# Kernel tuning notes

Measured on AMD Instinct MI355X. Metric: run time of the kernel, lower is better.

The kernel has to match this reference:

```python
import jax, jax.numpy as jnp
import numpy as np

N_FFT = 4096
HOP = 1024
WIN = 300          # wiener_win_len (frames per independent Wiener chunk)
EPS = 1e-10
SCALE_FACTOR = 10.0


def hann(n):
    # torch.hann_window (periodic)
    return 0.5 * (1.0 - jnp.cos(2.0 * jnp.pi * jnp.arange(n) / n))


def stft(x, window):
    # x: (N, C, T) -> complex (N, C, B, F), center=True, reflect pad, onesided
    pad = N_FFT // 2
    xp = jnp.pad(x, ((0, 0), (0, 0), (pad, pad)), mode='reflect')
    n_frames = 1 + (xp.shape[-1] - N_FFT) // HOP
    idx = jnp.arange(n_frames)[:, None] * HOP + jnp.arange(N_FFT)[None, :]
    frames = xp[..., idx] * window                      # (N,C,F,n_fft)
    spec = jnp.fft.rfft(frames, axis=-1)                # (N,C,F,B)
    return jnp.swapaxes(spec, -1, -2)                   # (N,C,B,F)


def istft(spec, window, length):
    # spec: (..., B, F) complex -> (..., length) real; center=True inverse
    frames = jnp.fft.irfft(jnp.swapaxes(spec, -1, -2), n=N_FFT, axis=-1) * window
    n_frames = frames.shape[-2]
    out_len = N_FFT + HOP * (n_frames - 1)
    idx = jnp.arange(n_frames)[:, None] * HOP + jnp.arange(N_FFT)[None, :]
    out = jnp.zeros(frames.shape[:-2] + (out_len,), frames.dtype).at[..., idx].add(frames)
    wsum = jnp.zeros((out_len,), frames.dtype).at[idx].add(
        jnp.broadcast_to(window ** 2, idx.shape))
    out = out / jnp.where(wsum > 1e-11, wsum, 1.0)
    pad = N_FFT // 2
    return out[..., pad:pad + length]


def wiener_chunk(v, x, niter):
    # openunmix.filtering.wiener (softmask=False, residual=False) on one chunk.
    # v: (T, B, C, S) real target magnitudes; x: (T, B, C) complex mix STFT.
    phase = jnp.exp(1j * jnp.angle(x))                  # mixture phase init
    y = (v * phase[..., None]).astype(jnp.complex64)    # (T,B,C,S)
    max_abs = jnp.maximum(1.0, jnp.max(jnp.abs(x)) / SCALE_FACTOR)
    x = x / max_abs
    y = y / max_abs
    C = x.shape[-1]
    reg = np.sqrt(EPS) * jnp.eye(C, dtype=jnp.complex64)
    for _ in range(niter):  # expectation_maximization, one pass per iter
        psd = jnp.mean(jnp.abs(y) ** 2, axis=2)         # (T,B,S) channel-avg PSD
        # spatial covariance per bin/source, normalized by eps + sum_t psd
        R = jnp.einsum('tbcs,tbds->bcds', y, jnp.conj(y))
        R = R / (EPS + jnp.sum(psd, axis=0))[:, None, None, :]
        Cxx = reg + jnp.einsum('tbs,bcds->tbcd', psd.astype(jnp.complex64), R)
        inv = jnp.linalg.inv(Cxx)                       # (T,B,C,C)
        gain = jnp.einsum('bacs,tbcd->tbads', R, inv) * psd[:, :, None, None, :]
        y = jnp.einsum('tbacs,tbc->tbas', gain, x)      # (T,B,C,S)
    return y * max_abs


def setup_inputs() -> dict:
    key = jax.random.key(0)
    k1, k2 = jax.random.split(key)
    audio = jax.random.normal(k1, (2, 2, 613376), dtype=jnp.float32)
    W = jax.random.normal(k2, (4, 2049), dtype=jnp.float32)  # per-target per-bin mask logits
    return {'audio': audio, 'W': W, 'niter': 1}


def reference(audio, W, niter):
    window = hann(N_FFT).astype(audio.dtype)
    mix = stft(audio, window)                           # (N,C,B,F) complex
    X = jnp.abs(mix)                                    # ComplexNorm power=1
    # target models (stand-in: per-bin sigmoid masks); input detached as in torch
    Xd = jax.lax.stop_gradient(X)
    masks = jax.nn.sigmoid(W)                           # (S,B)
    specs = Xd[..., None] * jnp.transpose(masks)[None, None, :, None, :]  # (N,C,B,F,S)
    v = jnp.transpose(specs, (0, 3, 2, 1, 4))           # (N,F,B,C,S)
    xm = jnp.transpose(mix, (0, 3, 2, 1))               # (N,F,B,C)
    N, F, B, C = xm.shape
    S = v.shape[-1]
    n_chunks = F // WIN
    vc = v.reshape(N, n_chunks, WIN, B, C, S)
    xc = xm.reshape(N, n_chunks, WIN, B, C)
    wfun = lambda vv, xx: wiener_chunk(vv, xx, niter)
    yc = jax.vmap(jax.vmap(wfun))(vc, xc)               # (N,chunks,T,B,C,S)
    y = yc.reshape(N, F, B, C, S)
    y = jnp.transpose(y, (0, 4, 3, 2, 1))               # (N,S,C,B,F)
    estimates = istft(y, window, audio.shape[-1])       # (N,S,C,T)
    return estimates
```

## Files before the change

### kernel.cpp

```cpp
#include <hip/hip_runtime.h>
#include <math.h>

#define TLEN 613376
#define OLEN 617472
#define NFR  600
#define NB   2049
#define PI_F  3.14159265358979323846f
#define PI2_F 6.28318530717958647693f
#define PHYS(i) ((i) + ((i) >> 4))

__device__ __forceinline__ float winf(int j) {
  return 0.5f - 0.5f * __cosf(1.5339807878856412e-3f * (float)j);
}

__device__ __forceinline__ float wsum_at(int m) {
  int f_max = m >> 10; if (f_max > 599) f_max = 599;
  int f_min = (m - 3072) >> 10; if (f_min < 0) f_min = 0;
  float ws = 0.f;
  for (int f2 = f_min; f2 <= f_max; ++f2) {
    float w = winf(m - (f2 << 10));
    ws += w * w;
  }
  return (ws > 1e-11f) ? ws : 1.0f;
}

__device__ __forceinline__ float reflect_load(const float* __restrict__ x, int pos) {
  int k = pos - 2048;
  if (k < 0) k = -k;
  else if (k >= TLEN) k = 2 * TLEN - 2 - k;
  return x[k];
}

__device__ __forceinline__ float2 cmul(float2 a, float2 b) {
  return make_float2(a.x * b.x - a.y * b.y, a.x * b.y + a.y * b.x);
}
__device__ __forceinline__ float2 cadd(float2 a, float2 b) { return make_float2(a.x + b.x, a.y + b.y); }
__device__ __forceinline__ float2 csub(float2 a, float2 b) { return make_float2(a.x - b.x, a.y - b.y); }
template<int SGN>
__device__ __forceinline__ float2 muli(float2 a) {
  return (SGN > 0) ? make_float2(-a.y, a.x) : make_float2(a.y, -a.x);
}

template<int SGN>
__device__ __forceinline__ void fft4(float2 v[4]) {
  float2 t0 = cadd(v[0], v[2]), t1 = csub(v[0], v[2]);
  float2 t2 = cadd(v[1], v[3]), t3 = csub(v[1], v[3]);
  float2 it3 = muli<SGN>(t3);
  v[0] = cadd(t0, t2); v[2] = csub(t0, t2);
  v[1] = cadd(t1, it3); v[3] = csub(t1, it3);
}

template<int SGN>
__device__ __forceinline__ void fft8(float2 v[8]) {
  const float C = 0.70710678118654752440f;
  const float s = (SGN > 0) ? 1.0f : -1.0f;
  float2 t0 = cadd(v[0], v[4]), t1 = csub(v[0], v[4]);
  float2 t2 = cadd(v[2], v[6]), t3 = csub(v[2], v[6]);
  float2 e0 = cadd(t0, t2), e2 = csub(t0, t2);
  float2 it3 = muli<SGN>(t3);
  float2 e1 = cadd(t1, it3), e3 = csub(t1, it3);
  t0 = cadd(v[1], v[5]); t1 = csub(v[1], v[5]);
  t2 = cadd(v[3], v[7]); t3 = csub(v[3], v[7]);
  float2 o0 = cadd(t0, t2), o2 = csub(t0, t2);
  it3 = muli<SGN>(t3);
  float2 o1 = cadd(t1, it3), o3 = csub(t1, it3);
  float2 o1w = make_float2(C * (o1.x - s * o1.y), C * (o1.y + s * o1.x));
  float2 o2w = muli<SGN>(o2);
  float2 o3w = make_float2(C * (-o3.x - s * o3.y), C * (-o3.y + s * o3.x));
  v[0] = cadd(e0, o0);  v[4] = csub(e0, o0);
  v[1] = cadd(e1, o1w); v[5] = csub(e1, o1w);
  v[2] = cadd(e2, o2w); v[6] = csub(e2, o2w);
  v[3] = cadd(e3, o3w); v[7] = csub(e3, o3w);
}

template<int SGN>
__device__ __forceinline__ void twiddle8(float2 v[8], float ang) {
  float sn, cs;
  __sincosf((SGN > 0) ? ang : -ang, &sn, &cs);
  float2 w1 = make_float2(cs, sn);
  float2 w = w1;
  v[1] = cmul(v[1], w);
#pragma unroll
  for (int r = 2; r < 8; ++r) { w = cmul(w, w1); v[r] = cmul(v[r], w); }
}

template<int SGN>
__device__ __forceinline__ void fft2048_mid(float2* lds, float2 v[8], int tid) {
  fft8<SGN>(v);
#pragma unroll
  for (int r = 0; r < 8; ++r) { int i = tid * 8 + r; lds[PHYS(i)] = v[r]; }
  __syncthreads();
#pragma unroll
  for (int r = 0; r < 8; ++r) v[r] = lds[PHYS(tid + 256 * r)];
  twiddle8<SGN>(v, PI2_F * (1.0f / 64.0f) * (float)(tid & 7));
  fft8<SGN>(v);
  __syncthreads();
#pragma unroll
  for (int r = 0; r < 8; ++r) { int i = ((tid >> 3) << 6) + (tid & 7) + 8 * r; lds[PHYS(i)] = v[r]; }
  __syncthreads();
#pragma unroll
  for (int r = 0; r < 8; ++r) v[r] = lds[PHYS(tid + 256 * r)];
  twiddle8<SGN>(v, PI2_F * (1.0f / 512.0f) * (float)(tid & 63));
  fft8<SGN>(v);
  __syncthreads();
#pragma unroll
  for (int r = 0; r < 8; ++r) { int i = ((tid >> 6) << 9) + (tid & 63) + 64 * r; lds[PHYS(i)] = v[r]; }
  __syncthreads();
}

template<int SGN>
__device__ __forceinline__ void fft2048_last(const float2* lds, int jj, float2 u[4]) {
#pragma unroll
  for (int r = 0; r < 4; ++r) u[r] = lds[PHYS(jj + 512 * r)];
  float sn, cs;
  float ang = PI2_F * (1.0f / 2048.0f) * (float)jj;
  __sincosf((SGN > 0) ? ang : -ang, &sn, &cs);
  float2 w1 = make_float2(cs, sn);
  float2 w2 = cmul(w1, w1);
  float2 w3 = cmul(w2, w1);
  u[1] = cmul(u[1], w1); u[2] = cmul(u[2], w2); u[3] = cmul(u[3], w3);
  fft4<SGN>(u);
}

__global__ __launch_bounds__(256, 6) void stft_kernel(const float* __restrict__ audio,
                                                      float2* __restrict__ X) {
  __shared__ float2 lds[2176];
  int bid = blockIdx.x;
  int w  = (bid & 7) * 300 + (bid >> 3);
  int f  = w % NFR;
  int nc = w / NFR;
  const float* x = audio + (size_t)nc * TLEN;
  int tid = threadIdx.x;
  int base = f * 1024;
  float2 v[8];
#pragma unroll
  for (int r = 0; r < 8; ++r) {
    int k = tid + 256 * r;
    int j0 = 2 * k;
    v[r] = make_float2(reflect_load(x, base + j0)     * winf(j0),
                       reflect_load(x, base + j0 + 1) * winf(j0 + 1));
  }
  fft2048_mid<-1>(lds, v, tid);
  fft2048_last<-1>(lds, tid,        v);
  fft2048_last<-1>(lds, tid + 256,  v + 4);
  __syncthreads();
#pragma unroll
  for (int r = 0; r < 4; ++r) lds[PHYS(tid + 512 * r)] = v[r];
#pragma unroll
  for (int r = 0; r < 4; ++r) lds[PHYS(tid + 256 + 512 * r)] = v[4 + r];
  __syncthreads();
  float2* out = X + ((size_t)nc * NFR + f) * NB;
  float sn0, cs0;
  __sincosf(-PI_F * (float)tid * (1.0f / 2048.0f), &sn0, &cs0);
  float2 ph = make_float2(cs0, sn0);
  const float2 rot = make_float2(0.92387953251128675613f, -0.38268343236508977173f);
#pragma unroll
  for (int r = 0; r < 9; ++r) {
    int k = tid + 256 * r;
    if (k <= 2048) {
      float2 Zk = lds[PHYS(k & 2047)];
      float2 Zm = lds[PHYS((2048 - k) & 2047)];
      float Ex = 0.5f * (Zk.x + Zm.x), Ey = 0.5f * (Zk.y - Zm.y);
      float Dx = 0.5f * (Zk.x - Zm.x), Dy = 0.5f * (Zk.y + Zm.y);
      float Ox = Dy, Oy = -Dx;
      out[k] = make_float2(Ex + Ox * ph.x - Oy * ph.y, Ey + Ox * ph.y + Oy * ph.x);
    }
    ph = cmul(ph, rot);
  }
}

__global__ __launch_bounds__(256) void stats_kernel(const float2* __restrict__ X,
                                                    float* __restrict__ stats4,
                                                    unsigned int* __restrict__ maxsq) {
  __shared__ unsigned int sm;
  if (threadIdx.x == 0) sm = 0u;
  __syncthreads();
  int b = blockIdx.x * 256 + threadIdx.x;
  bool ok = (b < NB);
  int g = blockIdx.y;
  int n = g >> 1, chunk = g & 1;
  int t0 = blockIdx.z * 75;
  const float2* X0 = X + ((size_t)(n * 2 + 0) * NFR + chunk * 300 + t0) * NB + (ok ? b : 0);
  const float2* X1 = X + ((size_t)(n * 2 + 1) * NFR + chunk * 300 + t0) * NB + (ok ? b : 0);
  float s00 = 0.f, s11 = 0.f, sre = 0.f, sim = 0.f, lmax = 0.f;
  if (ok) {
    for (int t = 0; t < 75; ++t) {
      float2 a = X0[(size_t)t * NB];
      float2 c = X1[(size_t)t * NB];
      float pa = a.x * a.x + a.y * a.y;
      float pc = c.x * c.x + c.y * c.y;
      s00 += pa; s11 += pc;
      sre += a.x * c.x + a.y * c.y;
      sim += a.y * c.x - a.x * c.y;
      lmax = fmaxf(lmax, fmaxf(pa, pc));
    }
  }
  atomicMax(&sm, __float_as_uint(lmax));
  __syncthreads();
  if (threadIdx.x == 0) atomicMax(&maxsq[g], sm);
  if (ok) {
    float* sp = stats4 + ((size_t)g * NB + b) * 4;
    unsafeAtomicAdd(sp + 0, s00);
    unsafeAtomicAdd(sp + 1, s11);
    unsafeAtomicAdd(sp + 2, sre);
    unsafeAtomicAdd(sp + 3, sim);
  }
}

__global__ __launch_bounds__(256) void alpha_kernel(const float* __restrict__ Wmask,
                                                    const float4* __restrict__ stats4,
                                                    const unsigned int* __restrict__ maxsq,
                                                    float* __restrict__ alpha,
                                                    float* __restrict__ Ksum) {
  int idx = blockIdx.x * 256 + threadIdx.x;
  if (idx >= 4 * NB) return;
  int b = idx % NB;
  int g = idx / NB;
  float ma2 = fmaxf(1.0f, __uint_as_float(maxsq[g]) * 0.01f);
  float4 s4 = stats4[(size_t)g * NB + b];
  float P = 0.5f * (s4.x + s4.y) / ma2;
  float K = 0.f;
#pragma unroll
  for (int s = 0; s < 4; ++s) {
    float mv = 1.0f / (1.0f + expf(-Wmask[s * NB + b]));
    float m2 = mv * mv;
    float a = (m2 * m2) / (1e-10f + m2 * P);
    alpha[(size_t)(g * 4 + s) * NB + b] = a;
    K += a;
  }
  Ksum[(size_t)g * NB + b] = K;
}

__global__ __launch_bounds__(256) void wiener_kernel(const float2* __restrict__ X,
                                                     const float4* __restrict__ stats4,
                                                     const float* __restrict__ Ksum,
                                                     const unsigned int* __restrict__ maxsq,
                                                     float2* __restrict__ Wc) {
  int idx = blockIdx.x * 256 + threadIdx.x;
  if (idx >= 4 * 300 * NB) return;
  int b = idx % NB;
  int gt = idx / NB;
  int t = gt % 300;
  int g = gt / 300;
  int n = g >> 1, chunk = g & 1;
  int f = chunk * 300 + t;
  float ima2 = 1.0f / fmaxf(1.0f, __uint_as_float(maxsq[g]) * 0.01f);
  float4 s4 = stats4[(size_t)g * NB + b];
  float g00 = s4.x * ima2, g11 = s4.y * ima2, gre = s4.z * ima2, gim = s4.w * ima2;
  float K = Ksum[(size_t)g * NB + b];
  float2 x0 = X[((size_t)(n * 2 + 0) * NFR + f) * NB + b];
  float2 x1 = X[((size_t)(n * 2 + 1) * NFR + f) * NB + b];
  float ph = 0.5f * ((x0.x * x0.x + x0.y * x0.y) + (x1.x * x1.x + x1.y * x1.y)) * ima2;
  float pk = ph * K;
  float M00 = 1e-5f + pk * g00;
  float M11 = 1e-5f + pk * g11;
  float Mre = pk * gre, Mim = pk * gim;
  float det = M00 * M11 - (Mre * Mre + Mim * Mim);
  float sc = ph / det;
  float u0x = M11 * x0.x - (Mre * x1.x - Mim * x1.y);
  float u0y = M11 * x0.y - (Mre * x1.y + Mim * x1.x);
  float u1x = M00 * x1.x - (Mre * x0.x + Mim * x0.y);
  float u1y = M00 * x1.y - (Mre * x0.y - Mim * x0.x);
  float w0x = g00 * u0x + (gre * u1x - gim * u1y);
  float w0y = g00 * u0y + (gre * u1y + gim * u1x);
  float w1x = (gre * u0x + gim * u0y) + g11 * u1x;
  float w1y = (gre * u0y - gim * u0x) + g11 * u1y;
  float2* out = Wc + ((size_t)(n * NFR + f) * 2) * NB + b;
  out[0]  = make_float2(w0x * sc, w0y * sc);
  out[NB] = make_float2(w1x * sc, w1y * sc);
}

template<int MODE>
__global__ __launch_bounds__(256, 6) void istft_pass_kernel(const float2* __restrict__ Wc,
                                                            const float* __restrict__ alpha,
                                                            float* __restrict__ accum,
                                                            float* __restrict__ out,
                                                            int pass) {
  __shared__ float2 lds[2176];
  int bid = blockIdx.x;
  int w = (bid & 7) * 300 + (bid >> 3);
  int member = w & 7;
  int grp = w >> 3;
  int fi = grp % 150;
  int n  = grp / 150;
  int s = member >> 1;
  int c = member & 1;
  int plane = n * 8 + s * 2 + c;
  int f = 4 * fi + pass;
  int g = n * 2 + (f >= 300 ? 1 : 0);
  int tid = threadIdx.x;
  const float2* Wrow = Wc + ((size_t)(n * NFR + f) * 2 + c) * NB;
  const float*  arow = alpha + (size_t)(g * 4 + s) * NB;
  float* acc = accum + (size_t)plane * OLEN + (size_t)f * 1024;

  float2 pre[8];
  if (MODE >= 1) {
#pragma unroll
    for (int half = 0; half < 2; ++half) {
#pragma unroll
      for (int r = 0; r < 4; ++r) {
        int m = tid + 256 * half + 512 * r;
        pre[half * 4 + r] = *(const float2*)&acc[2 * m];
      }
    }
  }

  float2 v[8];
  float sn0, cs0;
  __sincosf(PI_F * (float)tid * (1.0f / 2048.0f), &sn0, &cs0);
  float2 ph = make_float2(cs0, sn0);
  const float2 rot = make_float2(0.92387953251128675613f, 0.38268343236508977173f);
#pragma unroll
  for (int r = 0; r < 8; ++r) {
    int k = tid + 256 * r;
    float ak = arow[k];
    float2 sk = Wrow[k]; sk.x *= ak; sk.y *= ak;
    int rk = 2048 - k;
    float am = arow[rk];
    float2 sv = Wrow[rk]; sv.x *= am; sv.y *= am;
    float Ex = 0.5f * (sk.x + sv.x), Ey = 0.5f * (sk.y - sv.y);
    float Dx = 0.5f * (sk.x - sv.x), Dy = 0.5f * (sk.y + sv.y);
    float Ox = Dx * ph.x - Dy * ph.y, Oy = Dx * ph.y + Dy * ph.x;
    v[r] = make_float2(Ex - Oy, Ey + Ox);
    ph = cmul(ph, rot);
  }
  fft2048_mid<1>(lds, v, tid);
  float* outp = out + (size_t)plane * TLEN;
  const float scale = 1.0f / 2048.0f;
#pragma unroll
  for (int half = 0; half < 2; ++half) {
    int jj = tid + 256 * half;
    float2 u[4];
    fft2048_last<1>(lds, jj, u);
#pragma unroll
    for (int r = 0; r < 4; ++r) {
      int m = jj + 512 * r;
      int j0 = 2 * m;
      float2 val = make_float2(u[r].x * scale * winf(j0),
                               u[r].y * scale * winf(j0 + 1));
      float2* p = (float2*)&acc[j0];
      if (MODE == 0) {
        *p = val;
      } else if (MODE == 1) {
        float2 o = pre[half * 4 + r];
        val.x += o.x; val.y += o.y;
        *p = val;
      } else {
        int gm = f * 1024 + j0;
        if (gm < 615424) {
          float2 o = pre[half * 4 + r];
          val.x += o.x; val.y += o.y;
          float i0, i1;
          if (gm >= 3072 && gm + 1 < 614400) {
            i0 = 0.66666666666666667f; i1 = i0;
          } else {
            i0 = 1.0f / wsum_at(gm); i1 = 1.0f / wsum_at(gm + 1);
          }
          float2* po = (float2*)&outp[gm - 2048];
          *po = make_float2(val.x * i0, val.y * i1);
        }
      }
    }
  }
  if (MODE == 0 && fi == 149) {
    float* tail = accum + (size_t)plane * OLEN + 614400;
    for (int i = tid; i < OLEN - 614400; i += 256) tail[i] = 0.f;
  }
  if (MODE == 2 && fi == 0) {
    float* accp = accum + (size_t)plane * OLEN;
    for (int m = 2048 + tid; m < 3072; m += 256) {
      outp[m - 2048] = accp[m] / wsum_at(m);
    }
  }
}

extern "C" void kernel_launch(void* const* d_in, const int* in_sizes, int n_in,
                              void* d_out, int out_size, void* d_ws, size_t ws_size,
                              hipStream_t stream) {
  const float* audio = (const float*)d_in[0];
  const float* Wmask = (const float*)d_in[1];
  float* out = (float*)d_out;

  char* ws = (char*)d_ws;
  const size_t off_stats4 = 0;
  const size_t off_maxsq  = 131136;
  const size_t zero_span  = 131200;
  const size_t off_X      = zero_span;
  const size_t off_Wc     = off_X + 39340800;
  const size_t off_accum  = off_Wc + 39340800;
  const size_t off_alpha  = off_accum + 39518208;
  const size_t off_Ksum   = off_alpha + 131136;

  float*        stats4f = (float*)(ws + off_stats4);
  float4*       stats4  = (float4*)(ws + off_stats4);
  unsigned int* maxsq   = (unsigned int*)(ws + off_maxsq);
  float2*       X       = (float2*)(ws + off_X);
  float2*       Wc      = (float2*)(ws + off_Wc);
  float*        accum   = (float*)(ws + off_accum);
  float*        alpha   = (float*)(ws + off_alpha);
  float*        Ksum    = (float*)(ws + off_Ksum);

  hipMemsetAsync(ws, 0, zero_span, stream);

  stft_kernel<<<2400, 256, 0, stream>>>(audio, X);
  stats_kernel<<<dim3(9, 4, 4), 256, 0, stream>>>(X, stats4f, maxsq);
  alpha_kernel<<<(4 * NB + 255) / 256, 256, 0, stream>>>(Wmask, stats4, maxsq, alpha, Ksum);
  wiener_kernel<<<(4 * 300 * NB + 255) / 256, 256, 0, stream>>>(X, stats4, Ksum, maxsq, Wc);
  istft_pass_kernel<0><<<2400, 256, 0, stream>>>(Wc, alpha, accum, out, 0);
  istft_pass_kernel<1><<<2400, 256, 0, stream>>>(Wc, alpha, accum, out, 1);
  istft_pass_kernel<1><<<2400, 256, 0, stream>>>(Wc, alpha, accum, out, 2);
  istft_pass_kernel<2><<<2400, 256, 0, stream>>>(Wc, alpha, accum, out, 3);
}
```

Before: 199.1 us.

## Fuse Wiener filter evaluation into iSTFT passes, drop Wc intermediate buffer

Removes the standalone wiener_kernel and its ~39MB Wc intermediate. Each iSTFT block now recomputes the 2x2 Wiener solve per bin from X, stats4 and Ksum directly. This avoids writing and re-reading Wc through global memory and saves one launch. The cost is recomputation: the work for both channels is repeated per source (4x), which adds registers, so launch bounds drop to 4 waves and the loop unroll is reduced.

```diff
diff --git a/kernel.cpp b/kernel.cpp
--- a/kernel.cpp
+++ b/kernel.cpp
@@ -231,25 +231,17 @@
   Ksum[(size_t)g * NB + b] = K;
 }
 
-__global__ __launch_bounds__(256) void wiener_kernel(const float2* __restrict__ X,
-                                                     const float4* __restrict__ stats4,
-                                                     const float* __restrict__ Ksum,
-                                                     const unsigned int* __restrict__ maxsq,
-                                                     float2* __restrict__ Wc) {
-  int idx = blockIdx.x * 256 + threadIdx.x;
-  if (idx >= 4 * 300 * NB) return;
-  int b = idx % NB;
-  int gt = idx / NB;
-  int t = gt % 300;
-  int g = gt / 300;
-  int n = g >> 1, chunk = g & 1;
-  int f = chunk * 300 + t;
-  float ima2 = 1.0f / fmaxf(1.0f, __uint_as_float(maxsq[g]) * 0.01f);
-  float4 s4 = stats4[(size_t)g * NB + b];
+__device__ __forceinline__ float2 wiener_eval(int k, int c,
+                                              const float2* __restrict__ X0row,
+                                              const float2* __restrict__ X1row,
+                                              const float4* __restrict__ s4row,
+                                              const float* __restrict__ Krow,
+                                              float ima2) {
+  float4 s4 = s4row[k];
   float g00 = s4.x * ima2, g11 = s4.y * ima2, gre = s4.z * ima2, gim = s4.w * ima2;
-  float K = Ksum[(size_t)g * NB + b];
-  float2 x0 = X[((size_t)(n * 2 + 0) * NFR + f) * NB + b];
-  float2 x1 = X[((size_t)(n * 2 + 1) * NFR + f) * NB + b];
+  float K = Krow[k];
+  float2 x0 = X0row[k];
+  float2 x1 = X1row[k];
   float ph = 0.5f * ((x0.x * x0.x + x0.y * x0.y) + (x1.x * x1.x + x1.y * x1.y)) * ima2;
   float pk = ph * K;
   float M00 = 1e-5f + pk * g00;
@@ -261,17 +253,22 @@
   float u0y = M11 * x0.y - (Mre * x1.y + Mim * x1.x);
   float u1x = M00 * x1.x - (Mre * x0.x + Mim * x0.y);
   float u1y = M00 * x1.y - (Mre * x0.y - Mim * x0.x);
-  float w0x = g00 * u0x + (gre * u1x - gim * u1y);
-  float w0y = g00 * u0y + (gre * u1y + gim * u1x);
-  float w1x = (gre * u0x + gim * u0y) + g11 * u1x;
-  float w1y = (gre * u0y - gim * u0x) + g11 * u1y;
-  float2* out = Wc + ((size_t)(n * NFR + f) * 2) * NB + b;
-  out[0]  = make_float2(w0x * sc, w0y * sc);
-  out[NB] = make_float2(w1x * sc, w1y * sc);
+  float wx, wy;
+  if (c == 0) {
+    wx = g00 * u0x + (gre * u1x - gim * u1y);
+    wy = g00 * u0y + (gre * u1y + gim * u1x);
+  } else {
+    wx = (gre * u0x + gim * u0y) + g11 * u1x;
+    wy = (gre * u0y - gim * u0x) + g11 * u1y;
+  }
+  return make_float2(wx * sc, wy * sc);
 }
 
 template<int MODE>
-__global__ __launch_bounds__(256, 6) void istft_pass_kernel(const float2* __restrict__ Wc,
+__global__ __launch_bounds__(256, 4) void istft_pass_kernel(const float2* __restrict__ X,
+                                                            const float4* __restrict__ stats4,
+                                                            const float* __restrict__ Ksum,
+                                                            const unsigned int* __restrict__ maxsq,
                                                             const float* __restrict__ alpha,
                                                             float* __restrict__ accum,
                                                             float* __restrict__ out,
@@ -289,8 +286,12 @@
   int f = 4 * fi + pass;
   int g = n * 2 + (f >= 300 ? 1 : 0);
   int tid = threadIdx.x;
-  const float2* Wrow = Wc + ((size_t)(n * NFR + f) * 2 + c) * NB;
-  const float*  arow = alpha + (size_t)(g * 4 + s) * NB;
+  const float2* X0row = X + ((size_t)(n * 2 + 0) * NFR + f) * NB;
+  const float2* X1row = X + ((size_t)(n * 2 + 1) * NFR + f) * NB;
+  const float4* s4row = stats4 + (size_t)g * NB;
+  const float*  Krow  = Ksum + (size_t)g * NB;
+  const float*  arow  = alpha + (size_t)(g * 4 + s) * NB;
+  float ima2 = 1.0f / fmaxf(1.0f, __uint_as_float(maxsq[g]) * 0.01f);
   float* acc = accum + (size_t)plane * OLEN + (size_t)f * 1024;
 
   float2 pre[8];
@@ -310,14 +311,16 @@
   __sincosf(PI_F * (float)tid * (1.0f / 2048.0f), &sn0, &cs0);
   float2 ph = make_float2(cs0, sn0);
   const float2 rot = make_float2(0.92387953251128675613f, 0.38268343236508977173f);
-#pragma unroll
+#pragma unroll 4
   for (int r = 0; r < 8; ++r) {
     int k = tid + 256 * r;
     float ak = arow[k];
-    float2 sk = Wrow[k]; sk.x *= ak; sk.y *= ak;
+    float2 sk = wiener_eval(k, c, X0row, X1row, s4row, Krow, ima2);
+    sk.x *= ak; sk.y *= ak;
     int rk = 2048 - k;
     float am = arow[rk];
-    float2 sv = Wrow[rk]; sv.x *= am; sv.y *= am;
+    float2 sv = wiener_eval(rk, c, X0row, X1row, s4row, Krow, ima2);
+    sv.x *= am; sv.y *= am;
     float Ex = 0.5f * (sk.x + sv.x), Ey = 0.5f * (sk.y - sv.y);
     float Dx = 0.5f * (sk.x - sv.x), Dy = 0.5f * (sk.y + sv.y);
     float Ox = Dx * ph.x - Dy * ph.y, Oy = Dx * ph.y + Dy * ph.x;
@@ -386,8 +389,7 @@
   const size_t off_maxsq  = 131136;
   const size_t zero_span  = 131200;
   const size_t off_X      = zero_span;
-  const size_t off_Wc     = off_X + 39340800;
-  const size_t off_accum  = off_Wc + 39340800;
+  const size_t off_accum  = off_X + 39340800;
   const size_t off_alpha  = off_accum + 39518208;
   const size_t off_Ksum   = off_alpha + 131136;
 
@@ -395,7 +397,6 @@
   float4*       stats4  = (float4*)(ws + off_stats4);
   unsigned int* maxsq   = (unsigned int*)(ws + off_maxsq);
   float2*       X       = (float2*)(ws + off_X);
-  float2*       Wc      = (float2*)(ws + off_Wc);
   float*        accum   = (float*)(ws + off_accum);
   float*        alpha   = (float*)(ws + off_alpha);
   float*        Ksum    = (float*)(ws + off_Ksum);
@@ -405,9 +406,8 @@
   stft_kernel<<<2400, 256, 0, stream>>>(audio, X);
   stats_kernel<<<dim3(9, 4, 4), 256, 0, stream>>>(X, stats4f, maxsq);
   alpha_kernel<<<(4 * NB + 255) / 256, 256, 0, stream>>>(Wmask, stats4, maxsq, alpha, Ksum);
-  wiener_kernel<<<(4 * 300 * NB + 255) / 256, 256, 0, stream>>>(X, stats4, Ksum, maxsq, Wc);
-  istft_pass_kernel<0><<<2400, 256, 0, stream>>>(Wc, alpha, accum, out, 0);
-  istft_pass_kernel<1><<<2400, 256, 0, stream>>>(Wc, alpha, accum, out, 1);
-  istft_pass_kernel<1><<<2400, 256, 0, stream>>>(Wc, alpha, accum, out, 2);
-  istft_pass_kernel<2><<<2400, 256, 0, stream>>>(Wc, alpha, accum, out, 3);
-}
+  istft_pass_kernel<0><<<2400, 256, 0, stream>>>(X, stats4, Ksum, maxsq, alpha, accum, out, 0);
+  istft_pass_kernel<1><<<2400, 256, 0, stream>>>(X, stats4, Ksum, maxsq, alpha, accum, out, 1);
+  istft_pass_kernel<1><<<2400, 256, 0, stream>>>(X, stats4, Ksum, maxsq, alpha, accum, out, 2);
+  istft_pass_kernel<2><<<2400, 256, 0, stream>>>(X, stats4, Ksum, maxsq, alpha, accum, out, 3);
+}
```

After: 354.2 us. 77.9% more time.

## Replace four-pass iSTFT overlap-add with single atomic-add kernel

Applied to the files above, without the earlier changes.

Merges the four sequential iSTFT pass launches and the intermediate accumulation buffer into one kernel that applies window normalization per sample and atomically adds into a zeroed output. This removes the read-modify-write of the accum buffer, the extra launches and the edge-fixup logic. In exchange it adds a full output memset and two float atomics per output sample, with overlapping frames contending on the same addresses, and makes summation order nondeterministic.

```diff
diff --git a/kernel.cpp b/kernel.cpp
--- a/kernel.cpp
+++ b/kernel.cpp
@@ -2,7 +2,6 @@
 #include <math.h>
 
 #define TLEN 613376
-#define OLEN 617472
 #define NFR  600
 #define NB   2049
 #define PI_F  3.14159265358979323846f
@@ -270,17 +269,16 @@
   out[NB] = make_float2(w1x * sc, w1y * sc);
 }
 
-template<int MODE>
-__global__ __launch_bounds__(256, 6) void istft_pass_kernel(const float2* __restrict__ Wc,
-                                                            const float* __restrict__ alpha,
-                                                            float* __restrict__ accum,
-                                                            float* __restrict__ out,
-                                                            int pass) {
+__global__ __launch_bounds__(256, 6) void istft_atomic_kernel(const float2* __restrict__ Wc,
+                                                              const float* __restrict__ alpha,
+                                                              float* __restrict__ out) {
   __shared__ float2 lds[2176];
   int bid = blockIdx.x;
-  int w = (bid & 7) * 300 + (bid >> 3);
+  int w = (bid & 7) * 1200 + (bid >> 3);
   int member = w & 7;
-  int grp = w >> 3;
+  int rest = w >> 3;
+  int pass = rest & 3;
+  int grp = rest >> 2;
   int fi = grp % 150;
   int n  = grp / 150;
   int s = member >> 1;
@@ -291,19 +289,6 @@
   int tid = threadIdx.x;
   const float2* Wrow = Wc + ((size_t)(n * NFR + f) * 2 + c) * NB;
   const float*  arow = alpha + (size_t)(g * 4 + s) * NB;
-  float* acc = accum + (size_t)plane * OLEN + (size_t)f * 1024;
-
-  float2 pre[8];
-  if (MODE >= 1) {
-#pragma unroll
-    for (int half = 0; half < 2; ++half) {
-#pragma unroll
-      for (int r = 0; r < 4; ++r) {
-        int m = tid + 256 * half + 512 * r;
-        pre[half * 4 + r] = *(const float2*)&acc[2 * m];
-      }
-    }
-  }
 
   float2 v[8];
   float sn0, cs0;
@@ -336,40 +321,19 @@
     for (int r = 0; r < 4; ++r) {
       int m = jj + 512 * r;
       int j0 = 2 * m;
-      float2 val = make_float2(u[r].x * scale * winf(j0),
-                               u[r].y * scale * winf(j0 + 1));
-      float2* p = (float2*)&acc[j0];
-      if (MODE == 0) {
-        *p = val;
-      } else if (MODE == 1) {
-        float2 o = pre[half * 4 + r];
-        val.x += o.x; val.y += o.y;
-        *p = val;
-      } else {
-        int gm = f * 1024 + j0;
-        if (gm < 615424) {
-          float2 o = pre[half * 4 + r];
-          val.x += o.x; val.y += o.y;
-          float i0, i1;
-          if (gm >= 3072 && gm + 1 < 614400) {
-            i0 = 0.66666666666666667f; i1 = i0;
-          } else {
-            i0 = 1.0f / wsum_at(gm); i1 = 1.0f / wsum_at(gm + 1);
-          }
-          float2* po = (float2*)&outp[gm - 2048];
-          *po = make_float2(val.x * i0, val.y * i1);
+      int gm = f * 1024 + j0;
+      if (gm >= 2048 && gm < 615424) {
+        float i0, i1;
+        if (gm >= 3072 && gm + 1 < 614400) {
+          i0 = 0.66666666666666667f; i1 = i0;
+        } else {
+          i0 = 1.0f / wsum_at(gm); i1 = 1.0f / wsum_at(gm + 1);
         }
+        float vx = u[r].x * scale * winf(j0)     * i0;
+        float vy = u[r].y * scale * winf(j0 + 1) * i1;
+        unsafeAtomicAdd(&outp[gm - 2048], vx);
+        unsafeAtomicAdd(&outp[gm - 2047], vy);
       }
-    }
-  }
-  if (MODE == 0 && fi == 149) {
-    float* tail = accum + (size_t)plane * OLEN + 614400;
-    for (int i = tid; i < OLEN - 614400; i += 256) tail[i] = 0.f;
-  }
-  if (MODE == 2 && fi == 0) {
-    float* accp = accum + (size_t)plane * OLEN;
-    for (int m = 2048 + tid; m < 3072; m += 256) {
-      outp[m - 2048] = accp[m] / wsum_at(m);
     }
   }
 }
@@ -387,8 +351,7 @@
   const size_t zero_span  = 131200;
   const size_t off_X      = zero_span;
   const size_t off_Wc     = off_X + 39340800;
-  const size_t off_accum  = off_Wc + 39340800;
-  const size_t off_alpha  = off_accum + 39518208;
+  const size_t off_alpha  = off_Wc + 39340800;
   const size_t off_Ksum   = off_alpha + 131136;
 
   float*        stats4f = (float*)(ws + off_stats4);
@@ -396,18 +359,15 @@
   unsigned int* maxsq   = (unsigned int*)(ws + off_maxsq);
   float2*       X       = (float2*)(ws + off_X);
   float2*       Wc      = (float2*)(ws + off_Wc);
-  float*        accum   = (float*)(ws + off_accum);
   float*        alpha   = (float*)(ws + off_alpha);
   float*        Ksum    = (float*)(ws + off_Ksum);
 
   hipMemsetAsync(ws, 0, zero_span, stream);
+  hipMemsetAsync(d_out, 0, out_size, stream);
 
   stft_kernel<<<2400, 256, 0, stream>>>(audio, X);
   stats_kernel<<<dim3(9, 4, 4), 256, 0, stream>>>(X, stats4f, maxsq);
   alpha_kernel<<<(4 * NB + 255) / 256, 256, 0, stream>>>(Wmask, stats4, maxsq, alpha, Ksum);
   wiener_kernel<<<(4 * 300 * NB + 255) / 256, 256, 0, stream>>>(X, stats4, Ksum, maxsq, Wc);
-  istft_pass_kernel<0><<<2400, 256, 0, stream>>>(Wc, alpha, accum, out, 0);
-  istft_pass_kernel<1><<<2400, 256, 0, stream>>>(Wc, alpha, accum, out, 1);
-  istft_pass_kernel<1><<<2400, 256, 0, stream>>>(Wc, alpha, accum, out, 2);
-  istft_pass_kernel<2><<<2400, 256, 0, stream>>>(Wc, alpha, accum, out, 3);
-}
+  istft_atomic_kernel<<<9600, 256, 0, stream>>>(Wc, alpha, out);
+}
```

Result: slower. 368.7 us (+85.2%).
